# Kernel tuning notes

Hardware: AMD Instinct MI355X
Metric: run time of the kernel (lower is better)

The kernel has to match this reference:

```python
import jax, jax.numpy as jnp
import numpy as np

EPS = 1e-8
LN_EPS = 1e-5

def _layernorm(x, g, b):
    mu = jnp.mean(x, axis=-1, keepdims=True)
    var = jnp.mean((x - mu) ** 2, axis=-1, keepdims=True)
    return (x - mu) / jnp.sqrt(var + LN_EPS) * g + b

def setup_inputs() -> dict:
    key = jax.random.key(0)
    ks = jax.random.split(key, 10)
    B, S = 8192, 4096
    input_dim, hidden_dim = 4, 256
    h4 = hidden_dim // 4  # 64
    price_series = jax.random.uniform(ks[0], (B, S, 1), dtype=jnp.float32) + 0.5
    # 4 parallel encoders stacked on leading axis: Linear(input_dim->h4) + LayerNorm(h4)
    enc_w = jax.random.normal(ks[1], (4, input_dim, h4), dtype=jnp.float32) * 0.5
    enc_b = jax.random.normal(ks[2], (4, h4), dtype=jnp.float32) * 0.02
    enc_g = jnp.ones((4, h4), dtype=jnp.float32)
    enc_beta = jnp.zeros((4, h4), dtype=jnp.float32)
    # regime head: Linear(hidden_dim->64) + ReLU + (Dropout eval=identity) + Linear(64->4)
    head_w1 = jax.random.normal(ks[3], (hidden_dim, 64), dtype=jnp.float32) * 0.0625
    head_b1 = jnp.zeros((64,), dtype=jnp.float32)
    head_w2 = jax.random.normal(ks[4], (64, 4), dtype=jnp.float32) * 0.125
    head_b2 = jnp.zeros((4,), dtype=jnp.float32)
    return {"price_series": price_series, "enc_w": enc_w, "enc_b": enc_b,
            "enc_g": enc_g, "enc_beta": enc_beta,
            "head_w1": head_w1, "head_b1": head_b1,
            "head_w2": head_w2, "head_b2": head_b2}

def reference(price_series, enc_w, enc_b, enc_g, enc_beta, head_w1, head_b1, head_w2, head_b2):
    prices = price_series[:, :, 0]  # [B, S]
    B, S = prices.shape
    # Rolling SMA(20) with clamped window start, via cumsum (single pass, no per-step loop)
    csum = jnp.concatenate([jnp.zeros((B, 1), prices.dtype), jnp.cumsum(prices, axis=1)], axis=1)  # [B, S+1]
    i = jnp.arange(S)
    start20 = jnp.maximum(0, i - 19)
    cnt20 = (i - start20 + 1).astype(prices.dtype)
    sma20 = (csum[:, i + 1] - csum[:, start20]) / cnt20  # [B, S]
    trend_signal = (prices - sma20) / (sma20 + EPS)
    f_trend = jnp.mean(trend_signal, axis=1, keepdims=True)  # [B,1]
    # momentum over last 10 steps
    p_last = prices[:, -1:]
    p_m10 = prices[:, -10:-9]
    f_mom = (p_last - p_m10) / (p_m10 + EPS)  # [B,1]
    # mean reversion
    p_mean = jnp.mean(prices, axis=1, keepdims=True)
    f_mr = (p_last - p_mean) / (p_mean + EPS)  # [B,1]
    # cycle: coefficient of variation (torch.std is unbiased, ddof=1)
    f_cyc = jnp.std(prices, axis=1, ddof=1, keepdims=True) / (p_mean + EPS)  # [B,1]
    combined = jnp.concatenate([f_trend, f_mom, f_mr, f_cyc], axis=1)  # [B, 4]
    # 4 parallel encoders: Linear -> ReLU -> LayerNorm
    pre = jnp.einsum('bi,eio->ebo', combined, enc_w) + enc_b[:, None, :]  # [4, B, 64]
    feats = _layernorm(jax.nn.relu(pre), enc_g[:, None, :], enc_beta[:, None, :])  # [4, B, 64]
    # concat order: trend, momentum, mean_rev, cycle along feature dim
    regime_features = jnp.transpose(feats, (1, 0, 2)).reshape(B, -1)  # [B, 256]
    h = jax.nn.relu(regime_features @ head_w1 + head_b1)
    regime_probs = jax.nn.softmax(h @ head_w2 + head_b2, axis=1)  # [B, 4]
    return (regime_features, regime_probs)
```

## Files before the change

kernel.cpp:

```cpp
#include <hip/hip_runtime.h>

#define EPS 1e-8f
#define LN_EPS 1e-5f
#define NROWS 8192
#define SLEN 4096
#define PROBS_OFF 2097152

typedef __attribute__((ext_vector_type(8))) short bf16x8;
typedef __attribute__((ext_vector_type(4))) float f32x4;

__device__ __forceinline__ short f2bf(float f) {
    unsigned u = __float_as_uint(f);
    unsigned r = (u + 0x7FFFu + ((u >> 16) & 1u)) >> 16;
    return (short)r;
}

__global__ __launch_bounds__(256) void k_feat(const float* __restrict__ prices,
                                              float* __restrict__ comb) {
    const int t = threadIdx.x;
    const int lane = t & 63, wv = t >> 6;
    const int b = blockIdx.x * 4 + wv;
    const float* rowp = prices + (size_t)b * SLEN;
    const int p0 = lane * 64;

    float seg[64], prev[20];
    #pragma unroll
    for (int i = 0; i < 16; ++i)
        *(float4*)(seg + 4 * i) = *(const float4*)(rowp + p0 + 4 * i);
    #pragma unroll
    for (int i = 0; i < 5; ++i) {
        int base = p0 - 20 + 4 * i;
        float4 pv;
        if (base >= 0) pv = *(const float4*)(rowp + base);
        else pv = make_float4(0.f, 0.f, 0.f, 0.f);
        *(float4*)(prev + 4 * i) = pv;
    }

    float W = seg[0];
    #pragma unroll
    for (int j = 1; j < 20; ++j) W += prev[j];

    float x = seg[0];
    float sum = x, sq = x * x;
    float cnt = fminf((float)(p0 + 1), 20.0f);
    float sma = W * __builtin_amdgcn_rcpf(cnt);
    float ts = (x - sma) * __builtin_amdgcn_rcpf(sma + EPS);
    #pragma unroll
    for (int j = 1; j < 64; ++j) {
        x = seg[j];
        float old = (j < 20) ? prev[j] : seg[j - 20];
        W += x - old;
        sum += x;
        sq = fmaf(x, x, sq);
        float c2 = fminf((float)(p0 + j + 1), 20.0f);
        float sm = W * __builtin_amdgcn_rcpf(c2);
        ts += (x - sm) * __builtin_amdgcn_rcpf(sm + EPS);
    }

    #pragma unroll
    for (int off = 32; off > 0; off >>= 1) {
        sum += __shfl_xor(sum, off);
        sq  += __shfl_xor(sq,  off);
        ts  += __shfl_xor(ts,  off);
    }
    float p_last = __shfl(seg[63], 63);
    float p_m10  = __shfl(seg[54], 63);

    if (lane == 0) {
        float mean = sum * (1.0f / 4096.0f);
        float var  = fmaxf((sq - 4096.0f * mean * mean) * (1.0f / 4095.0f), 0.0f);
        float4 c;
        c.x = ts * (1.0f / 4096.0f);
        c.y = (p_last - p_m10) / (p_m10 + EPS);
        c.z = (p_last - mean) / (mean + EPS);
        c.w = sqrtf(var) / (mean + EPS);
        *(float4*)(comb + (size_t)b * 4) = c;
    }
}

#define ROWS 32

__global__ __launch_bounds__(256) void k_head(
    const float* __restrict__ combg, float* __restrict__ out,
    const float* __restrict__ enc_w, const float* __restrict__ enc_b,
    const float* __restrict__ enc_g, const float* __restrict__ enc_bt,
    const float* __restrict__ w1, const float* __restrict__ b1,
    const float* __restrict__ w2, const float* __restrict__ b2)
{
    __shared__ float comb[ROWS][4];
    __shared__ short rfb[ROWS][264];
    __shared__ float hbuf[ROWS][68];

    const int t = threadIdx.x;
    const int r0 = blockIdx.x * ROWS;
    const int lane = t & 63, wave = t >> 6;
    const int l15 = lane & 15, q = lane >> 4;

    if (t < ROWS * 4)
        comb[t >> 2][t & 3] = combg[(size_t)(r0 + (t >> 2)) * 4 + (t & 3)];

    bf16x8 bfrag[8];
    #pragma unroll
    for (int kt = 0; kt < 8; ++kt) {
        #pragma unroll
        for (int j = 0; j < 8; ++j) {
            int k = kt * 32 + q * 8 + j;
            bfrag[kt][j] = f2bf(w1[k * 64 + wave * 16 + l15]);
        }
    }

    const float ew0 = enc_w[wave * 256 + lane];
    const float ew1v = enc_w[wave * 256 + 64 + lane];
    const float ew2v = enc_w[wave * 256 + 128 + lane];
    const float ew3v = enc_w[wave * 256 + 192 + lane];
    const float ebv = enc_b[t], egv = enc_g[t], btv = enc_bt[t];

    __syncthreads();

    for (int r = 0; r < ROWS; ++r) {
        float4 cb = *(const float4*)comb[r];
        float v = fmaf(cb.x, ew0, fmaf(cb.y, ew1v, fmaf(cb.z, ew2v, fmaf(cb.w, ew3v, ebv))));
        v = fmaxf(v, 0.0f);
        float sm = v;
        #pragma unroll
        for (int off = 32; off > 0; off >>= 1) sm += __shfl_xor(sm, off);
        float mu = sm * (1.0f / 64.0f);
        float d = v - mu;
        float vs = d * d;
        #pragma unroll
        for (int off = 32; off > 0; off >>= 1) vs += __shfl_xor(vs, off);
        float y = fmaf(d * rsqrtf(vs * (1.0f / 64.0f) + LN_EPS), egv, btv);
        out[(size_t)(r0 + r) * 256 + t] = y;
        rfb[r][t] = f2bf(y);
    }
    __syncthreads();

    f32x4 acc0 = {0.f, 0.f, 0.f, 0.f}, acc1 = {0.f, 0.f, 0.f, 0.f};
    #pragma unroll
    for (int kt = 0; kt < 8; ++kt) {
        bf16x8 a0 = *(const bf16x8*)&rfb[l15][kt * 32 + q * 8];
        bf16x8 a1 = *(const bf16x8*)&rfb[16 + l15][kt * 32 + q * 8];
        acc0 = __builtin_amdgcn_mfma_f32_16x16x32_bf16(a0, bfrag[kt], acc0, 0, 0, 0);
        acc1 = __builtin_amdgcn_mfma_f32_16x16x32_bf16(a1, bfrag[kt], acc1, 0, 0, 0);
    }

    const int col = wave * 16 + l15;
    const float b1v = b1[col];
    #pragma unroll
    for (int rg = 0; rg < 4; ++rg) {
        hbuf[q * 4 + rg][col]      = fmaxf(acc0[rg] + b1v, 0.0f);
        hbuf[16 + q * 4 + rg][col] = fmaxf(acc1[rg] + b1v, 0.0f);
    }
    __syncthreads();

    if (t < 128) {
        int r = t >> 2, c = t & 3;
        float lg = b2[c];
        #pragma unroll
        for (int j = 0; j < 64; ++j) lg = fmaf(hbuf[r][j], w2[j * 4 + c], lg);
        float mx = fmaxf(lg, __shfl_xor(lg, 1, 4));
        mx = fmaxf(mx, __shfl_xor(mx, 2, 4));
        float ex = __expf(lg - mx);
        float s2 = ex + __shfl_xor(ex, 1, 4);
        s2 += __shfl_xor(s2, 2, 4);
        out[PROBS_OFF + (size_t)(r0 + r) * 4 + c] = ex / s2;
    }
}

extern "C" void kernel_launch(void* const* d_in, const int* in_sizes, int n_in,
                              void* d_out, int out_size, void* d_ws, size_t ws_size,
                              hipStream_t stream) {
    const float* prices  = (const float*)d_in[0];
    const float* enc_w   = (const float*)d_in[1];
    const float* enc_b   = (const float*)d_in[2];
    const float* enc_g   = (const float*)d_in[3];
    const float* enc_bt  = (const float*)d_in[4];
    const float* head_w1 = (const float*)d_in[5];
    const float* head_b1 = (const float*)d_in[6];
    const float* head_w2 = (const float*)d_in[7];
    const float* head_b2 = (const float*)d_in[8];
    float* out  = (float*)d_out;
    float* comb = (float*)d_ws;

    k_feat<<<NROWS / 4, 256, 0, stream>>>(prices, comb);
    k_head<<<NROWS / ROWS, 256, 0, stream>>>(comb, out, enc_w, enc_b, enc_g, enc_bt,
                                             head_w1, head_b1, head_w2, head_b2);
}
```

Baseline: 227.8 us.

## Process one row per block via LDS staging in feature kernel

```diff
diff --git a/kernel.cpp b/kernel.cpp
--- a/kernel.cpp
+++ b/kernel.cpp
@@ -17,43 +17,49 @@
 
 __global__ __launch_bounds__(256) void k_feat(const float* __restrict__ prices,
                                               float* __restrict__ comb) {
+    __shared__ float sld[SLEN + (SLEN >> 4)];
+    __shared__ float red[12];
+
     const int t = threadIdx.x;
+    const int b = blockIdx.x;
     const int lane = t & 63, wv = t >> 6;
-    const int b = blockIdx.x * 4 + wv;
-    const float* rowp = prices + (size_t)b * SLEN;
-    const int p0 = lane * 64;
-
-    float seg[64], prev[20];
-    #pragma unroll
-    for (int i = 0; i < 16; ++i)
-        *(float4*)(seg + 4 * i) = *(const float4*)(rowp + p0 + 4 * i);
-    #pragma unroll
-    for (int i = 0; i < 5; ++i) {
-        int base = p0 - 20 + 4 * i;
-        float4 pv;
-        if (base >= 0) pv = *(const float4*)(rowp + base);
-        else pv = make_float4(0.f, 0.f, 0.f, 0.f);
-        *(float4*)(prev + 4 * i) = pv;
-    }
-
-    float W = seg[0];
-    #pragma unroll
-    for (int j = 1; j < 20; ++j) W += prev[j];
-
-    float x = seg[0];
-    float sum = x, sq = x * x;
-    float cnt = fminf((float)(p0 + 1), 20.0f);
-    float sma = W * __builtin_amdgcn_rcpf(cnt);
-    float ts = (x - sma) * __builtin_amdgcn_rcpf(sma + EPS);
-    #pragma unroll
-    for (int j = 1; j < 64; ++j) {
-        x = seg[j];
-        float old = (j < 20) ? prev[j] : seg[j - 20];
-        W += x - old;
+    const float4* rowp4 = (const float4*)(prices + (size_t)b * SLEN);
+
+#define SL(i) sld[(i) + ((i) >> 4)]
+
+    #pragma unroll
+    for (int i = 0; i < 4; ++i) {
+        float4 v = rowp4[i * 256 + t];
+        int idx = (i * 256 + t) * 4;
+        int a = idx + (idx >> 4);
+        sld[a] = v.x; sld[a + 1] = v.y; sld[a + 2] = v.z; sld[a + 3] = v.w;
+    }
+    __syncthreads();
+
+    const int p0 = t * 16;
+    float W = 0.0f;
+    #pragma unroll
+    for (int jj = 1; jj < 20; ++jj) {
+        int oi = p0 - 20 + jj;
+        float pv = SL(oi < 0 ? 0 : oi);
+        W += (oi >= 0) ? pv : 0.0f;
+    }
+
+    float sum = 0.0f, sq = 0.0f, ts = 0.0f;
+    #pragma unroll
+    for (int j = 0; j < 16; ++j) {
+        float x = SL(p0 + j);
+        if (j == 0) {
+            W += x;
+        } else {
+            int oi = p0 + j - 20;
+            float ov = SL(oi < 0 ? 0 : oi);
+            W += x - ((oi >= 0) ? ov : 0.0f);
+        }
         sum += x;
         sq = fmaf(x, x, sq);
-        float c2 = fminf((float)(p0 + j + 1), 20.0f);
-        float sm = W * __builtin_amdgcn_rcpf(c2);
+        float c = fminf((float)(p0 + j + 1), 20.0f);
+        float sm = W * __builtin_amdgcn_rcpf(c);
         ts += (x - sm) * __builtin_amdgcn_rcpf(sm + EPS);
     }
 
@@ -63,19 +69,25 @@
         sq  += __shfl_xor(sq,  off);
         ts  += __shfl_xor(ts,  off);
     }
-    float p_last = __shfl(seg[63], 63);
-    float p_m10  = __shfl(seg[54], 63);
-
-    if (lane == 0) {
-        float mean = sum * (1.0f / 4096.0f);
-        float var  = fmaxf((sq - 4096.0f * mean * mean) * (1.0f / 4095.0f), 0.0f);
+    if (lane == 0) { red[wv * 3] = sum; red[wv * 3 + 1] = sq; red[wv * 3 + 2] = ts; }
+    __syncthreads();
+
+    if (t == 0) {
+        float S = red[0] + red[3] + red[6] + red[9];
+        float Q = red[1] + red[4] + red[7] + red[10];
+        float T = red[2] + red[5] + red[8] + red[11];
+        float mean = S * (1.0f / 4096.0f);
+        float var  = fmaxf((Q - 4096.0f * mean * mean) * (1.0f / 4095.0f), 0.0f);
+        float p_last = SL(4095);
+        float p_m10  = SL(4086);
         float4 c;
-        c.x = ts * (1.0f / 4096.0f);
+        c.x = T * (1.0f / 4096.0f);
         c.y = (p_last - p_m10) / (p_m10 + EPS);
         c.z = (p_last - mean) / (mean + EPS);
         c.w = sqrtf(var) / (mean + EPS);
         *(float4*)(comb + (size_t)b * 4) = c;
     }
+#undef SL
 }
 
 #define ROWS 32
@@ -182,7 +194,7 @@
     float* out  = (float*)d_out;
     float* comb = (float*)d_ws;
 
-    k_feat<<<NROWS / 4, 256, 0, stream>>>(prices, comb);
+    k_feat<<<NROWS, 256, 0, stream>>>(prices, comb);
     k_head<<<NROWS / ROWS, 256, 0, stream>>>(comb, out, enc_w, enc_b, enc_g, enc_bt,
                                              head_w1, head_b1, head_w2, head_b2);
 }
```

Result: faster. 222.6 us (-2.3%).
